# Performance work log

Measured on AMD Instinct MI355X. Metric: run time of the kernel, lower is better.

## Reference

```python
import jax, jax.numpy as jnp
import numpy as np

EPS = 1e-5
QB = 127.0  # 2**(8-1) - 1


def absmean_quantize(w):
    """Ternary quantization (BitNet b1.58): gamma = mean|W|, W_q in {-1,0,1}."""
    gamma = jnp.mean(jnp.abs(w))
    u = w / jnp.maximum(gamma, EPS)
    w_q = jnp.clip(jnp.round(u), -1.0, 1.0)
    return w_q, gamma


def absmax_quantize(x, bits=8):
    """Per-token int8 absmax quantization: alpha = max|x| over last dim."""
    qb = float(2 ** (bits - 1) - 1)
    alpha = jnp.max(jnp.abs(x), axis=-1, keepdims=True)  # [..., 1]
    u = x * qb / jnp.maximum(alpha, EPS)
    x_q = jnp.clip(jnp.round(u), -qb, qb)
    return x_q, alpha


def setup_inputs() -> dict:
    key = jax.random.key(0)
    k1, k2 = jax.random.split(key)
    B, S, D_IN, D_OUT = 4, 2048, 2048, 8192
    x = jax.random.normal(k1, (B, S, D_IN), dtype=jnp.float32)
    # kaiming-uniform-ish init scale for weight [out, in]
    bound = 1.0 / np.sqrt(D_IN)
    weight = jax.random.uniform(k2, (D_OUT, D_IN), minval=-bound, maxval=bound, dtype=jnp.float32)
    return {"x": x, "weight": weight}


def reference(x, weight):
    w_q, gamma = absmean_quantize(weight)          # [O,I], scalar
    x_q, alpha = absmax_quantize(x, bits=8)        # [B,S,I], [B,S,1]
    out = jnp.einsum('bsi,oi->bso', x_q, w_q)      # float matmul of quantized values
    scale = alpha * gamma / QB                     # [B,S,1]
    return out * scale
```

## Files before the change

kernel.cpp:

```cpp
#include <hip/hip_runtime.h>
#include <hip/hip_bf16.h>
#include <stdint.h>

typedef int i32x4 __attribute__((ext_vector_type(4)));
typedef float f32x4 __attribute__((ext_vector_type(4)));

#define K_DIM 2048
#define M_DIM 8192
#define N_DIM 8192
#define QBF   127.0f
#define EPSF  1e-5f
#define NT    32

__device__ __forceinline__ void load_lds16(const void* gsrc, void* ldst) {
    __builtin_amdgcn_global_load_lds(
        (__attribute__((address_space(1))) void*)gsrc,
        (__attribute__((address_space(3))) void*)ldst,
        16, 0, 0);
}

__global__ __launch_bounds__(256) void k_abs_partial(const float* __restrict__ w,
                                                     float* __restrict__ partial) {
    __shared__ float red[256];
    int t = threadIdx.x, b = blockIdx.x;
    const float4* w4 = (const float4*)w;
    size_t base = (size_t)b * 2048;
    float s = 0.f;
#pragma unroll
    for (int j = 0; j < 8; ++j) {
        float4 v = w4[base + j * 256 + t];
        s += fabsf(v.x) + fabsf(v.y) + fabsf(v.z) + fabsf(v.w);
    }
    red[t] = s; __syncthreads();
    for (int off = 128; off > 0; off >>= 1) {
        if (t < off) red[t] += red[t + off];
        __syncthreads();
    }
    if (t == 0) partial[b] = red[0];
}

__global__ __launch_bounds__(256) void k_gamma(const float* __restrict__ partial,
                                               float* __restrict__ gamma) {
    __shared__ float red[256];
    int t = threadIdx.x;
    float s = 0.f;
#pragma unroll
    for (int j = 0; j < 8; ++j) s += partial[t + j * 256];
    red[t] = s; __syncthreads();
    for (int off = 128; off > 0; off >>= 1) {
        if (t < off) red[t] += red[t + off];
        __syncthreads();
    }
    if (t == 0) gamma[0] = red[0] / 16777216.0f;
}

__global__ __launch_bounds__(256) void k_quant_w(const float* __restrict__ w,
                                                 const float* __restrict__ gamma,
                                                 uint* __restrict__ wq) {
    float g = fmaxf(gamma[0], EPSF);
    int tid = blockIdx.x * 256 + threadIdx.x;
    float4 v = ((const float4*)w)[tid];
    int a = (int)fminf(fmaxf(rintf(v.x / g), -1.f), 1.f);
    int b = (int)fminf(fmaxf(rintf(v.y / g), -1.f), 1.f);
    int c = (int)fminf(fmaxf(rintf(v.z / g), -1.f), 1.f);
    int d = (int)fminf(fmaxf(rintf(v.w / g), -1.f), 1.f);
    wq[tid] = (a & 255) | ((b & 255) << 8) | ((c & 255) << 16) | ((d & 255) << 24);
}

__global__ __launch_bounds__(256) void k_quant_x(const float* __restrict__ x,
                                                 uint* __restrict__ xq,
                                                 float* __restrict__ alpha) {
    __shared__ float red[256];
    int t = threadIdx.x, row = blockIdx.x;
    const float4* x4 = (const float4*)x + (size_t)row * 512;
    float4 v0 = x4[t], v1 = x4[t + 256];
    float m = fmaxf(fmaxf(fabsf(v0.x), fabsf(v0.y)), fmaxf(fabsf(v0.z), fabsf(v0.w)));
    m = fmaxf(m, fmaxf(fmaxf(fabsf(v1.x), fabsf(v1.y)), fmaxf(fabsf(v1.z), fabsf(v1.w))));
    red[t] = m; __syncthreads();
    for (int off = 128; off > 0; off >>= 1) {
        if (t < off) red[t] = fmaxf(red[t], red[t + off]);
        __syncthreads();
    }
    float a = red[0];
    if (t == 0) alpha[row] = a;
    float den = fmaxf(a, EPSF);
    uint* q = xq + (size_t)row * 512;
    int q0 = (int)fminf(fmaxf(rintf(v0.x * QBF / den), -QBF), QBF);
    int q1 = (int)fminf(fmaxf(rintf(v0.y * QBF / den), -QBF), QBF);
    int q2 = (int)fminf(fmaxf(rintf(v0.z * QBF / den), -QBF), QBF);
    int q3 = (int)fminf(fmaxf(rintf(v0.w * QBF / den), -QBF), QBF);
    q[t] = (q0 & 255) | ((q1 & 255) << 8) | ((q2 & 255) << 16) | ((q3 & 255) << 24);
    q0 = (int)fminf(fmaxf(rintf(v1.x * QBF / den), -QBF), QBF);
    q1 = (int)fminf(fmaxf(rintf(v1.y * QBF / den), -QBF), QBF);
    q2 = (int)fminf(fmaxf(rintf(v1.z * QBF / den), -QBF), QBF);
    q3 = (int)fminf(fmaxf(rintf(v1.w * QBF / den), -QBF), QBF);
    q[t + 256] = (q0 & 255) | ((q1 & 255) << 8) | ((q2 & 255) << 16) | ((q3 & 255) << 24);
}

__global__ __launch_bounds__(512, 2) void k_gemm(const uint8_t* __restrict__ xq,
                                                 const uint8_t* __restrict__ wq,
                                                 const float* __restrict__ alpha,
                                                 const float* __restrict__ gamma,
                                                 float* __restrict__ out) {
    __shared__ __align__(16) char smem[98304];

    int bid = blockIdx.x;
    int wg = (bid & 7) * 128 + (bid >> 3);
    int tm = wg >> 5, tn = wg & 31;

    int t = threadIdx.x;
    int w = t >> 6, l = t & 63;
    int wr = w >> 2, wc = w & 3;

    const uint8_t* srcb[4];
    int dstq[4];
    {
        int rsub = l >> 2;
        int clog = (l & 3) ^ ((rsub >> 1) & 3);
#pragma unroll
        for (int j = 0; j < 4; ++j) {
            int q = w * 4 + j;
            int isB = q >> 4;
            int r = (q & 15) * 16 + rsub;
            int grow = (isB ? tn : tm) * 256 + r;
            srcb[j] = (isB ? wq : xq) + (size_t)grow * K_DIM + clog * 16;
            dstq[j] = q * 1024;
        }
    }

    i32x4 acc[8][4];
#pragma unroll
    for (int m = 0; m < 8; ++m)
#pragma unroll
        for (int n = 0; n < 4; ++n) acc[m][n] = (i32x4){0, 0, 0, 0};

    int lrow = l & 15, kgrp = l >> 4;
    int cph = (kgrp ^ ((lrow >> 1) & 3)) * 16;
    int aoff[8], boff[4];
#pragma unroll
    for (int mf = 0; mf < 8; ++mf) aoff[mf] = (wr * 128 + mf * 16 + lrow) * 64 + cph;
#pragma unroll
    for (int nf = 0; nf < 4; ++nf) boff[nf] = 16384 + (wc * 64 + nf * 16 + lrow) * 64 + cph;

#pragma unroll
    for (int p = 0; p < 2; ++p)
#pragma unroll
        for (int j = 0; j < 4; ++j)
            load_lds16(srcb[j] + (size_t)p * 64, smem + p * 32768 + dstq[j]);
    asm volatile("s_waitcnt vmcnt(4)" ::: "memory");
    __builtin_amdgcn_s_barrier();

    int slot = 0;
    for (int kt = 0; kt < NT; ++kt) {
        char* sb = smem + slot * 32768;
        int ds = slot + 2; if (ds >= 3) ds -= 3;
        char* db = smem + ds * 32768;
        bool pf = (kt + 2 < NT);
        i32x4 a[8], b[4];

#pragma unroll
        for (int nf = 0; nf < 4; ++nf) b[nf] = *(const i32x4*)(sb + boff[nf]);
#pragma unroll
        for (int mf = 0; mf < 4; ++mf) a[mf] = *(const i32x4*)(sb + aoff[mf]);
        if (pf) {
            load_lds16(srcb[0] + (size_t)(kt + 2) * 64, db + dstq[0]);
            load_lds16(srcb[1] + (size_t)(kt + 2) * 64, db + dstq[1]);
        }
        __builtin_amdgcn_s_barrier();
        asm volatile("s_waitcnt lgkmcnt(0)" ::: "memory");
        __builtin_amdgcn_sched_barrier(0);
        __builtin_amdgcn_s_setprio(1);
#pragma unroll
        for (int mf = 0; mf < 4; ++mf)
#pragma unroll
            for (int nf = 0; nf < 4; ++nf)
                acc[mf][nf] = __builtin_amdgcn_mfma_i32_16x16x64_i8(
                    a[mf], b[nf], acc[mf][nf], 0, 0, 0);
        __builtin_amdgcn_s_setprio(0);
        __builtin_amdgcn_s_barrier();

#pragma unroll
        for (int mf = 4; mf < 8; ++mf) a[mf] = *(const i32x4*)(sb + aoff[mf]);
        if (pf) {
            load_lds16(srcb[2] + (size_t)(kt + 2) * 64, db + dstq[2]);
            load_lds16(srcb[3] + (size_t)(kt + 2) * 64, db + dstq[3]);
        }
        __builtin_amdgcn_s_barrier();
        asm volatile("s_waitcnt lgkmcnt(0)" ::: "memory");
        __builtin_amdgcn_sched_barrier(0);
        __builtin_amdgcn_s_setprio(1);
#pragma unroll
        for (int mf = 4; mf < 8; ++mf)
#pragma unroll
            for (int nf = 0; nf < 4; ++nf)
                acc[mf][nf] = __builtin_amdgcn_mfma_i32_16x16x64_i8(
                    a[mf], b[nf], acc[mf][nf], 0, 0, 0);
        __builtin_amdgcn_s_setprio(0);
        if (kt < NT - 2) asm volatile("s_waitcnt vmcnt(4)" ::: "memory");
        else             asm volatile("s_waitcnt vmcnt(0)" ::: "memory");
        __builtin_amdgcn_s_barrier();

        slot = (slot == 2) ? 0 : slot + 1;
    }

    asm volatile("s_waitcnt lgkmcnt(0)" ::: "memory");
    __builtin_amdgcn_s_barrier();
    float gs = gamma[0] / QBF;
    int orow0 = tm * 256 + wr * 128;
    int ocol0 = tn * 256 + wc * 64;
    int kgrp4 = kgrp * 4;
    char* ebase = smem + w * 8704;
#pragma unroll
    for (int mf = 0; mf < 8; ++mf) {
        float* eb = (float*)(ebase + (mf & 1) * 4352);
        int rbase = orow0 + mf * 16;
#pragma unroll
        for (int reg = 0; reg < 4; ++reg) {
            float s = alpha[rbase + kgrp4 + reg] * gs;
            int rowo = (kgrp4 + reg) * 68;
#pragma unroll
            for (int nf = 0; nf < 4; ++nf)
                eb[rowo + nf * 16 + lrow] = (float)acc[mf][nf][reg] * s;
        }
        asm volatile("s_waitcnt lgkmcnt(0)" ::: "memory");
        __builtin_amdgcn_sched_barrier(0);
#pragma unroll
        for (int pass = 0; pass < 4; ++pass) {
            int r16 = (pass >> 1) * 8 + (l >> 3);
            int fc  = (pass & 1) * 8 + (l & 7);
            f32x4 v = *(const f32x4*)(eb + r16 * 68 + fc * 4);
            __builtin_nontemporal_store(
                v, (f32x4*)(out + (size_t)(rbase + r16) * N_DIM + ocol0 + fc * 4));
        }
        asm volatile("s_waitcnt lgkmcnt(0)" ::: "memory");
        __builtin_amdgcn_sched_barrier(0);
    }
}

extern "C" void kernel_launch(void* const* d_in, const int* in_sizes, int n_in,
                              void* d_out, int out_size, void* d_ws, size_t ws_size,
                              hipStream_t stream) {
    const float* x  = (const float*)d_in[0];
    const float* wt = (const float*)d_in[1];
    float* out = (float*)d_out;

    char* ws = (char*)d_ws;
    uint8_t* xq     = (uint8_t*)ws;
    uint8_t* wq     = (uint8_t*)(ws + 16777216);
    float* alpha    = (float*)(ws + 33554432);
    float* partial  = (float*)(ws + 33587200);
    float* gamma    = (float*)(ws + 33595392);

    k_abs_partial<<<2048, 256, 0, stream>>>(wt, partial);
    k_gamma<<<1, 256, 0, stream>>>(partial, gamma);
    k_quant_w<<<16384, 256, 0, stream>>>(wt, gamma, (uint*)wq);
    k_quant_x<<<8192, 256, 0, stream>>>(x, (uint*)xq, alpha);
    k_gemm<<<1024, 512, 0, stream>>>(xq, wq, alpha, gamma, out);
}
```

Measured before the change: 202.1 us.

## Pre-pack ternary weights into MFMA fragment layout and load B directly to registers

The weight quantization kernel now writes int8 weights in a layout that matches the MFMA B-operand fragments, so each lane can fetch its 16-byte B fragment with a plain global load. The GEMM stops staging B through LDS: it double-buffers B in registers, prefetching one k-step ahead, and keeps only A in a three-slot LDS ring. This shrinks LDS use and LDS traffic and removes some barriers. In exchange, each wave issues uncached-style global loads for B that are not shared across waves in the same row, and the vmcnt bookkeeping becomes more intricate.

```diff
diff --git a/kernel.cpp b/kernel.cpp
--- a/kernel.cpp
+++ b/kernel.cpp
@@ -56,7 +56,7 @@
 
 __global__ __launch_bounds__(256) void k_quant_w(const float* __restrict__ w,
                                                  const float* __restrict__ gamma,
-                                                 uint* __restrict__ wq) {
+                                                 uint* __restrict__ wq_p) {
     float g = fmaxf(gamma[0], EPSF);
     int tid = blockIdx.x * 256 + threadIdx.x;
     float4 v = ((const float4*)w)[tid];
@@ -64,7 +64,12 @@
     int b = (int)fminf(fmaxf(rintf(v.y / g), -1.f), 1.f);
     int c = (int)fminf(fmaxf(rintf(v.z / g), -1.f), 1.f);
     int d = (int)fminf(fmaxf(rintf(v.w / g), -1.f), 1.f);
-    wq[tid] = (a & 255) | ((b & 255) << 8) | ((c & 255) << 16) | ((d & 255) << 24);
+    uint word = (a & 255) | ((b & 255) << 8) | ((c & 255) << 16) | ((d & 255) << 24);
+    int n = tid >> 9, k4 = tid & 511;
+    int kt = k4 >> 4, chunk = (k4 >> 2) & 3, wrd = k4 & 3;
+    int l = (n & 15) | (chunk << 4);
+    int gidx = (n >> 4) * 2048 + kt * 64 + l;
+    wq_p[gidx * 4 + wrd] = word;
 }
 
 __global__ __launch_bounds__(256) void k_quant_x(const float* __restrict__ x,
@@ -98,11 +103,11 @@
 }
 
 __global__ __launch_bounds__(512, 2) void k_gemm(const uint8_t* __restrict__ xq,
-                                                 const uint8_t* __restrict__ wq,
+                                                 const uint8_t* __restrict__ wq_p,
                                                  const float* __restrict__ alpha,
                                                  const float* __restrict__ gamma,
                                                  float* __restrict__ out) {
-    __shared__ __align__(16) char smem[98304];
+    __shared__ __align__(16) char smem[73728];
 
     int bid = blockIdx.x;
     int wg = (bid & 7) * 128 + (bid >> 3);
@@ -112,22 +117,25 @@
     int w = t >> 6, l = t & 63;
     int wr = w >> 2, wc = w & 3;
 
-    const uint8_t* srcb[4];
-    int dstq[4];
+    const uint8_t* srcb[2];
+    int dstq[2];
     {
         int rsub = l >> 2;
         int clog = (l & 3) ^ ((rsub >> 1) & 3);
 #pragma unroll
-        for (int j = 0; j < 4; ++j) {
-            int q = w * 4 + j;
-            int isB = q >> 4;
-            int r = (q & 15) * 16 + rsub;
-            int grow = (isB ? tn : tm) * 256 + r;
-            srcb[j] = (isB ? wq : xq) + (size_t)grow * K_DIM + clog * 16;
+        for (int j = 0; j < 2; ++j) {
+            int q = w * 2 + j;
+            int r = q * 16 + rsub;
+            srcb[j] = xq + (size_t)(tm * 256 + r) * K_DIM + clog * 16;
             dstq[j] = q * 1024;
         }
     }
 
+    const uint8_t* bptr[4];
+#pragma unroll
+    for (int nf = 0; nf < 4; ++nf)
+        bptr[nf] = wq_p + (size_t)(tn * 16 + wc * 4 + nf) * 32768 + l * 16;
+
     i32x4 acc[8][4];
 #pragma unroll
     for (int m = 0; m < 8; ++m)
@@ -136,72 +144,79 @@
 
     int lrow = l & 15, kgrp = l >> 4;
     int cph = (kgrp ^ ((lrow >> 1) & 3)) * 16;
-    int aoff[8], boff[4];
+    int aoff[8];
 #pragma unroll
     for (int mf = 0; mf < 8; ++mf) aoff[mf] = (wr * 128 + mf * 16 + lrow) * 64 + cph;
-#pragma unroll
-    for (int nf = 0; nf < 4; ++nf) boff[nf] = 16384 + (wc * 64 + nf * 16 + lrow) * 64 + cph;
-
-#pragma unroll
-    for (int p = 0; p < 2; ++p)
-#pragma unroll
-        for (int j = 0; j < 4; ++j)
-            load_lds16(srcb[j] + (size_t)p * 64, smem + p * 32768 + dstq[j]);
-    asm volatile("s_waitcnt vmcnt(4)" ::: "memory");
-    __builtin_amdgcn_s_barrier();
+
+    i32x4 bE[4], bO[4];
+
+    load_lds16(srcb[0], smem + dstq[0]);
+    load_lds16(srcb[1], smem + dstq[1]);
+    load_lds16(srcb[0] + 64, smem + 16384 + dstq[0]);
+    load_lds16(srcb[1] + 64, smem + 16384 + dstq[1]);
+    __builtin_amdgcn_sched_barrier(0);
+#pragma unroll
+    for (int nf = 0; nf < 4; ++nf) bE[nf] = *(const i32x4*)(bptr[nf]);
+    __builtin_amdgcn_sched_barrier(0);
 
     int slot = 0;
-    for (int kt = 0; kt < NT; ++kt) {
-        char* sb = smem + slot * 32768;
-        int ds = slot + 2; if (ds >= 3) ds -= 3;
-        char* db = smem + ds * 32768;
-        bool pf = (kt + 2 < NT);
-        i32x4 a[8], b[4];
-
-#pragma unroll
-        for (int nf = 0; nf < 4; ++nf) b[nf] = *(const i32x4*)(sb + boff[nf]);
-#pragma unroll
-        for (int mf = 0; mf < 4; ++mf) a[mf] = *(const i32x4*)(sb + aoff[mf]);
-        if (pf) {
-            load_lds16(srcb[0] + (size_t)(kt + 2) * 64, db + dstq[0]);
-            load_lds16(srcb[1] + (size_t)(kt + 2) * 64, db + dstq[1]);
-        }
-        __builtin_amdgcn_s_barrier();
-        asm volatile("s_waitcnt lgkmcnt(0)" ::: "memory");
-        __builtin_amdgcn_sched_barrier(0);
-        __builtin_amdgcn_s_setprio(1);
-#pragma unroll
-        for (int mf = 0; mf < 4; ++mf)
-#pragma unroll
-            for (int nf = 0; nf < 4; ++nf)
-                acc[mf][nf] = __builtin_amdgcn_mfma_i32_16x16x64_i8(
-                    a[mf], b[nf], acc[mf][nf], 0, 0, 0);
-        __builtin_amdgcn_s_setprio(0);
-        __builtin_amdgcn_s_barrier();
-
-#pragma unroll
-        for (int mf = 4; mf < 8; ++mf) a[mf] = *(const i32x4*)(sb + aoff[mf]);
-        if (pf) {
-            load_lds16(srcb[2] + (size_t)(kt + 2) * 64, db + dstq[2]);
-            load_lds16(srcb[3] + (size_t)(kt + 2) * 64, db + dstq[3]);
-        }
-        __builtin_amdgcn_s_barrier();
-        asm volatile("s_waitcnt lgkmcnt(0)" ::: "memory");
-        __builtin_amdgcn_sched_barrier(0);
-        __builtin_amdgcn_s_setprio(1);
-#pragma unroll
-        for (int mf = 4; mf < 8; ++mf)
-#pragma unroll
-            for (int nf = 0; nf < 4; ++nf)
-                acc[mf][nf] = __builtin_amdgcn_mfma_i32_16x16x64_i8(
-                    a[mf], b[nf], acc[mf][nf], 0, 0, 0);
-        __builtin_amdgcn_s_setprio(0);
-        if (kt < NT - 2) asm volatile("s_waitcnt vmcnt(4)" ::: "memory");
-        else             asm volatile("s_waitcnt vmcnt(0)" ::: "memory");
-        __builtin_amdgcn_s_barrier();
-
-        slot = (slot == 2) ? 0 : slot + 1;
-    }
+#define ITER(KT, BC, BN)                                                         \
+    {                                                                            \
+        if ((KT) < NT - 1) asm volatile("s_waitcnt vmcnt(6)" ::: "memory");      \
+        else               asm volatile("s_waitcnt vmcnt(4)" ::: "memory");      \
+        __builtin_amdgcn_s_barrier();                                            \
+        char* sb = smem + slot * 16384;                                          \
+        int ds = slot + 2; if (ds >= 3) ds -= 3;                                 \
+        i32x4 a[8];                                                              \
+        _Pragma("unroll")                                                        \
+        for (int mf = 0; mf < 4; ++mf) a[mf] = *(const i32x4*)(sb + aoff[mf]);   \
+        __builtin_amdgcn_sched_barrier(0);                                       \
+        _Pragma("unroll")                                                        \
+        for (int mf = 4; mf < 8; ++mf) a[mf] = *(const i32x4*)(sb + aoff[mf]);   \
+        __builtin_amdgcn_sched_barrier(0);                                       \
+        if ((KT) + 2 < NT) {                                                     \
+            char* db = smem + ds * 16384;                                        \
+            load_lds16(srcb[0] + (size_t)((KT) + 2) * 64, db + dstq[0]);         \
+            load_lds16(srcb[1] + (size_t)((KT) + 2) * 64, db + dstq[1]);         \
+        }                                                                        \
+        __builtin_amdgcn_sched_barrier(0);                                       \
+        if ((KT) + 1 < NT) {                                                     \
+            _Pragma("unroll")                                                    \
+            for (int nf = 0; nf < 4; ++nf)                                       \
+                BN[nf] = *(const i32x4*)(bptr[nf] + (size_t)((KT) + 1) * 1024);  \
+        }                                                                        \
+        __builtin_amdgcn_sched_barrier(0);                                       \
+        if ((KT) <= NT - 3)      asm volatile("s_waitcnt vmcnt(6)" ::: "memory");\
+        else if ((KT) == NT - 2) asm volatile("s_waitcnt vmcnt(4)" ::: "memory");\
+        else                     asm volatile("s_waitcnt vmcnt(0)" ::: "memory");\
+        asm volatile("s_waitcnt lgkmcnt(4)" ::: "memory");                       \
+        __builtin_amdgcn_sched_barrier(0);                                       \
+        __builtin_amdgcn_s_setprio(1);                                           \
+        _Pragma("unroll")                                                        \
+        for (int mf = 0; mf < 4; ++mf)                                           \
+            _Pragma("unroll")                                                    \
+            for (int nf = 0; nf < 4; ++nf)                                       \
+                acc[mf][nf] = __builtin_amdgcn_mfma_i32_16x16x64_i8(             \
+                    a[mf], BC[nf], acc[mf][nf], 0, 0, 0);                        \
+        __builtin_amdgcn_s_setprio(0);                                           \
+        asm volatile("s_waitcnt lgkmcnt(0)" ::: "memory");                       \
+        __builtin_amdgcn_sched_barrier(0);                                       \
+        __builtin_amdgcn_s_setprio(1);                                           \
+        _Pragma("unroll")                                                        \
+        for (int mf = 4; mf < 8; ++mf)                                           \
+            _Pragma("unroll")                                                    \
+            for (int nf = 0; nf < 4; ++nf)                                       \
+                acc[mf][nf] = __builtin_amdgcn_mfma_i32_16x16x64_i8(             \
+                    a[mf], BC[nf], acc[mf][nf], 0, 0, 0);                        \
+        __builtin_amdgcn_s_setprio(0);                                           \
+        slot = (slot == 2) ? 0 : slot + 1;                                       \
+    }
+
+    for (int kt = 0; kt < NT; kt += 2) {
+        ITER(kt,     bE, bO)
+        ITER(kt + 1, bO, bE)
+    }
+#undef ITER
 
     asm volatile("s_waitcnt lgkmcnt(0)" ::: "memory");
     __builtin_amdgcn_s_barrier();
@@ -246,14 +261,14 @@
 
     char* ws = (char*)d_ws;
     uint8_t* xq     = (uint8_t*)ws;
-    uint8_t* wq     = (uint8_t*)(ws + 16777216);
+    uint8_t* wq_p   = (uint8_t*)(ws + 16777216);
     float* alpha    = (float*)(ws + 33554432);
     float* partial  = (float*)(ws + 33587200);
     float* gamma    = (float*)(ws + 33595392);
 
     k_abs_partial<<<2048, 256, 0, stream>>>(wt, partial);
     k_gamma<<<1, 256, 0, stream>>>(partial, gamma);
-    k_quant_w<<<16384, 256, 0, stream>>>(wt, gamma, (uint*)wq);
+    k_quant_w<<<16384, 256, 0, stream>>>(wt, gamma, (uint*)wq_p);
     k_quant_x<<<8192, 256, 0, stream>>>(x, (uint*)xq, alpha);
-    k_gemm<<<1024, 512, 0, stream>>>(xq, wq, alpha, gamma, out);
-}
+    k_gemm<<<1024, 512, 0, stream>>>(xq, wq_p, alpha, gamma, out);
+}
```

Result: slower. 221.0 us (+9.3%).
